# Kernel tuning notes

Hardware: AMD Instinct MI355X
Metric: run time of the kernel (lower is better)

Reference implementation:

```python
import jax, jax.numpy as jnp
import numpy as np

INF = 100000000.0
TOPK = 27


def _box_iou(a, b):
    # a: [N,4] (x1,y1,x2,y2), b: [G,4] -> iou [N,G]
    area_a = (a[:, 2] - a[:, 0]) * (a[:, 3] - a[:, 1])
    area_b = (b[:, 2] - b[:, 0]) * (b[:, 3] - b[:, 1])
    lt = jnp.maximum(a[:, None, :2], b[None, :, :2])
    rb = jnp.minimum(a[:, None, 2:], b[None, :, 2:])
    wh = jnp.clip(rb - lt, 0.0)
    inter = wh[..., 0] * wh[..., 1]
    union = area_a[:, None] + area_b[None, :] - inter
    return inter / union, union


def _assign_one(anchors, gts, tokens):
    # anchors [N,4], gts [G,4], tokens [G,T]
    N = anchors.shape[0]
    G = gts.shape[0]
    ious, _ = _box_iou(anchors, gts)  # [N,G]

    a_cx = (anchors[:, 2] + anchors[:, 0]) * 0.5
    a_cy = (anchors[:, 3] + anchors[:, 1]) * 0.5
    g_cx = (gts[:, 2] + gts[:, 0]) * 0.5
    g_cy = (gts[:, 3] + gts[:, 1]) * 0.5

    # pairwise center distance [N,G]
    dist = jnp.sqrt((a_cx[:, None] - g_cx[None, :]) ** 2 +
                    (a_cy[:, None] - g_cy[None, :]) ** 2)

    # topk nearest anchors per gt (smallest distance) -> idxs [G,TOPK]
    _, topk_idxs = jax.lax.top_k(-dist.T, TOPK)

    # candidate ious [G,TOPK]
    cand = jnp.take_along_axis(ious.T, topk_idxs, axis=1)
    iou_mean = cand.mean(axis=1)
    iou_std = cand.std(axis=1, ddof=1)  # torch.std is unbiased
    is_pos = cand >= (iou_mean + iou_std)[:, None]

    # center-inside-gt check [G,TOPK]
    ax = a_cx[topk_idxs]
    ay = a_cy[topk_idxs]
    l = ax - gts[:, 0:1]
    t = ay - gts[:, 1:2]
    r = gts[:, 2:3] - ax
    b = gts[:, 3:4] - ay
    is_in_gts = jnp.minimum(jnp.minimum(l, t), jnp.minimum(r, b)) > 0.01
    is_pos = is_pos & is_in_gts

    # scatter candidate ious into flat [G*N] buffer of -INF (indices are unique)
    flat_idx = (jnp.arange(G)[:, None] * N + topk_idxs).reshape(-1)
    vals = ious.T.reshape(-1)[flat_idx]
    scat = jnp.where(is_pos.reshape(-1), vals, -INF)
    ious_inf = jnp.full((G * N,), -INF, dtype=ious.dtype).at[flat_idx].set(scat)
    ious_inf = ious_inf.reshape(G, N).T  # [N,G]

    anchors_to_gt_values = ious_inf.max(axis=1)          # [N]
    anchors_to_gt_indexs = ious_inf.argmax(axis=1)       # [N]

    matched_gts = gts[anchors_to_gt_indexs]              # [N,4]

    T = tokens.shape[1]
    unmatched = jnp.zeros((T,), tokens.dtype).at[-1].set(1.0)
    token_labels = jnp.where((anchors_to_gt_values == -INF)[:, None],
                             unmatched[None, :],
                             tokens[anchors_to_gt_indexs])  # [N,T]
    return anchors_to_gt_values, anchors_to_gt_indexs, matched_gts, token_labels


def setup_inputs() -> dict:
    key = jax.random.key(0)
    k1, k2, k3, k4, k5 = jax.random.split(key, 5)
    B, N, G, T = 8, 100000, 64, 256
    # anchors: valid x1<x2, y1<y2 boxes on a ~1024px canvas
    a_c = jax.random.uniform(k1, (B, N, 2), jnp.float32, 0.0, 1024.0)
    a_wh = jax.random.uniform(k2, (B, N, 2), jnp.float32, 8.0, 128.0)
    anchor_boxes = jnp.concatenate([a_c - a_wh / 2, a_c + a_wh / 2], axis=-1)
    g_c = jax.random.uniform(k3, (B, G, 2), jnp.float32, 0.0, 1024.0)
    g_wh = jax.random.uniform(k4, (B, G, 2), jnp.float32, 64.0, 512.0)
    gt_boxes = jnp.concatenate([g_c - g_wh / 2, g_c + g_wh / 2], axis=-1)
    token_map = jax.random.uniform(k5, (B, G, T), jnp.float32)
    return {"anchor_boxes": anchor_boxes, "gt_boxes": gt_boxes,
            "token_map": token_map}


def reference(anchor_boxes, gt_boxes, token_map):
    return jax.vmap(_assign_one)(anchor_boxes, gt_boxes, token_map)
```

## Files before the change

kernel.cpp:

```cpp
#include <hip/hip_runtime.h>
#include <cstdint>

constexpr int B = 8, N = 100000, G = 64, T = 256, TOPK = 27;
constexpr int BN = B * N;
constexpr int CAP = 1536;
constexpr int GPB = 2;
constexpr int TOKEN_BLOCKS = 2048;
#define NEG_INF_VAL (-100000000.0f)

typedef float v4f __attribute__((ext_vector_type(4)));

__global__ __launch_bounds__(256) void atss_centers_kernel(
    const float* __restrict__ anchors, float2* __restrict__ ctr,
    unsigned long long* __restrict__ best)
{
#pragma clang fp contract(off)
  int i = blockIdx.x * 256 + threadIdx.x;
  if (i < BN) {
    float4 ab = ((const float4*)anchors)[i];
    ctr[i] = make_float2((ab.z + ab.x) * 0.5f, (ab.w + ab.y) * 0.5f);
    best[i] = 0ULL;
  }
}

__global__ __launch_bounds__(1024) void atss_assign_kernel(
    const float* __restrict__ anchors,
    const float2* __restrict__ ctr,
    const float* __restrict__ gts,
    unsigned long long* __restrict__ best)
{
#pragma clang fp contract(off)
  __shared__ float s_d[GPB][CAP];
  __shared__ int   s_i[GPB][CAP];
  __shared__ int   s_cnt[GPB];
  __shared__ int   s_sel[GPB][TOPK];
  __shared__ float s_iou[GPB][TOPK];
  __shared__ int   s_in[GPB][TOPK];
  __shared__ float s_thresh;

  const int bid = blockIdx.x;
  const int p   = (bid & 7) * 32 + (bid >> 3);
  const int b   = p >> 5;
  const int g0  = (p & 31) * 2;
  const int bg0 = b * G + g0;
  const int tid = threadIdx.x;

  const float4 gb0 = ((const float4*)gts)[bg0];
  const float4 gb1 = ((const float4*)gts)[bg0 + 1];
  const float gcx0 = (gb0.z + gb0.x) * 0.5f, gcy0 = (gb0.w + gb0.y) * 0.5f;
  const float gcx1 = (gb1.z + gb1.x) * 0.5f, gcy1 = (gb1.w + gb1.y) * 0.5f;

  const float4* abase = (const float4*)(anchors + (size_t)b * N * 4);
  const float4* c4    = (const float4*)(ctr + (size_t)b * N);

  float thr2_0 = 576.0f, thr2_1 = 576.0f;
  int M0 = -1, M1 = -1;
  for (int attempt = 0; attempt < 8 && (M0 < 0 || M1 < 0); ++attempt) {
    if (tid == 0 && M0 < 0) s_cnt[0] = 0;
    if (tid == 1 && M1 < 0) s_cnt[1] = 0;
    __syncthreads();
    const bool a0 = (M0 < 0), a1 = (M1 < 0);

#define ATSS_TEST(cx, cy, idx)                                                \
  do {                                                                        \
    if (a0) {                                                                 \
      float dx = (cx) - gcx0, dy = (cy) - gcy0;                               \
      float d2 = __fmul_rn(dx, dx) + __fmul_rn(dy, dy);                       \
      if (d2 < thr2_0) {                                                      \
        int q_ = atomicAdd(&s_cnt[0], 1);                                     \
        if (q_ < CAP) { s_d[0][q_] = __fsqrt_rn(d2); s_i[0][q_] = (idx); }    \
      }                                                                       \
    }                                                                         \
    if (a1) {                                                                 \
      float dx = (cx) - gcx1, dy = (cy) - gcy1;                               \
      float d2 = __fmul_rn(dx, dx) + __fmul_rn(dy, dy);                       \
      if (d2 < thr2_1) {                                                      \
        int q_ = atomicAdd(&s_cnt[1], 1);                                     \
        if (q_ < CAP) { s_d[1][q_] = __fsqrt_rn(d2); s_i[1][q_] = (idx); }    \
      }                                                                       \
    }                                                                         \
  } while (0)

    for (int m = tid; m < N / 4; m += 1024) {
      float4 ca = c4[2 * m];
      float4 cb = c4[2 * m + 1];
      ATSS_TEST(ca.x, ca.y, 4 * m);
      ATSS_TEST(ca.z, ca.w, 4 * m + 1);
      ATSS_TEST(cb.x, cb.y, 4 * m + 2);
      ATSS_TEST(cb.z, cb.w, 4 * m + 3);
    }
#undef ATSS_TEST
    __syncthreads();
    const int c0 = s_cnt[0], c1 = s_cnt[1];
    __syncthreads();
    if (M0 < 0) {
      if (c0 >= TOPK && c0 <= CAP) M0 = c0;
      else thr2_0 *= (c0 < TOPK) ? 16.0f : 0.25f;
    }
    if (M1 < 0) {
      if (c1 >= TOPK && c1 <= CAP) M1 = c1;
      else thr2_1 *= (c1 < TOPK) ? 16.0f : 0.25f;
    }
  }

  for (int q = 0; q < GPB; ++q) {
    const int M = (q == 0) ? M0 : M1;
    const float4 gbox = (q == 0) ? gb0 : gb1;
    const int g = g0 + q;

    for (int s = tid; s < M; s += 1024) {
      unsigned long long pk_s =
          ((unsigned long long)__float_as_uint(s_d[q][s]) << 20) |
          (unsigned long long)(unsigned)s_i[q][s];
      int rank = 0;
      for (int j = 0; j < M; ++j) {
        unsigned long long pk_j =
            ((unsigned long long)__float_as_uint(s_d[q][j]) << 20) |
            (unsigned long long)(unsigned)s_i[q][j];
        rank += (pk_j < pk_s) ? 1 : 0;
      }
      if (rank < TOPK) s_sel[q][rank] = s_i[q][s];
    }
    __syncthreads();

    if (tid < TOPK) {
      int a = s_sel[q][tid];
      float4 ab = abase[a];
      float area_a = __fmul_rn(ab.z - ab.x, ab.w - ab.y);
      float area_b = __fmul_rn(gbox.z - gbox.x, gbox.w - gbox.y);
      float ltx = fmaxf(ab.x, gbox.x), lty = fmaxf(ab.y, gbox.y);
      float rbx = fminf(ab.z, gbox.z), rby = fminf(ab.w, gbox.w);
      float w = fmaxf(rbx - ltx, 0.0f), h = fmaxf(rby - lty, 0.0f);
      float inter = __fmul_rn(w, h);
      float uni = (area_a + area_b) - inter;
      s_iou[q][tid] = inter / uni;
      float acx = (ab.z + ab.x) * 0.5f, acy = (ab.w + ab.y) * 0.5f;
      float l = acx - gbox.x, t = acy - gbox.y;
      float r = gbox.z - acx, bt = gbox.w - acy;
      float mn = fminf(fminf(l, t), fminf(r, bt));
      s_in[q][tid] = (mn > 0.01f) ? 1 : 0;
    }
    __syncthreads();

    if (tid == 0) {
      float sum = 0.0f;
      for (int k = 0; k < TOPK; ++k) sum += s_iou[q][k];
      float mean = sum / (float)TOPK;
      float vs = 0.0f;
      for (int k = 0; k < TOPK; ++k) {
        float d = s_iou[q][k] - mean;
        vs += __fmul_rn(d, d);
      }
      float sd = __fsqrt_rn(vs / (float)(TOPK - 1));
      s_thresh = mean + sd;
    }
    __syncthreads();

    if (tid < TOPK) {
      float iou = s_iou[q][tid];
      if (s_in[q][tid] && iou >= s_thresh) {
        unsigned long long pk =
            ((unsigned long long)__float_as_uint(iou) << 32) |
            (unsigned long long)(0xFFFFFFFFu - (unsigned)g);
        atomicMax(&best[(size_t)b * N + s_sel[q][tid]], pk);
      }
    }
    __syncthreads();
  }
}

__global__ __launch_bounds__(256) void atss_scalar_write_kernel(
    const unsigned long long* __restrict__ best,
    const float* __restrict__ gts,
    float* __restrict__ out)
{
  float* __restrict__ out_val = out;
  float* __restrict__ out_idx = out + (size_t)BN;
  float* __restrict__ out_mg  = out + (size_t)2 * BN;

  const int i = blockIdx.x * 256 + threadIdx.x;
  unsigned long long p = best[i];
  const int b_ = i / N;
  int g = 0;
  float val = NEG_INF_VAL;
  if (p != 0ULL) {
    g   = (int)(0xFFFFFFFFu - (unsigned)(p & 0xFFFFFFFFULL));
    val = __uint_as_float((unsigned)(p >> 32));
  }
  const int row = b_ * G + g;
  out_val[i] = val;
  out_idx[i] = (float)g;
  ((v4f*)out_mg)[i] = ((const v4f*)gts)[row];
}

__global__ __launch_bounds__(256) void atss_token_kernel(
    const unsigned long long* __restrict__ best,
    const float* __restrict__ tokens,
    float* __restrict__ out)
{
  float* __restrict__ out_tok = out + (size_t)6 * BN;
  const int lane = threadIdx.x & 63;
  const int NW   = TOKEN_BLOCKS * 4;
  int row = (blockIdx.x << 2) | (threadIdx.x >> 6);
  const v4f* tok4 = (const v4f*)tokens;

  unsigned long long p = best[row];
  while (true) {
    const int nrow = row + NW;
    unsigned long long pn = (nrow < BN) ? best[nrow] : 0ULL;
    v4f t;
    if (p != 0ULL) {
      const int b_ = row / N;
      const int g  = (int)(0xFFFFFFFFu - (unsigned)(p & 0xFFFFFFFFULL));
      t = tok4[(size_t)(b_ * G + g) * 64 + lane];
    } else {
      t = (v4f){0.0f, 0.0f, 0.0f, 0.0f};
      if (lane == 63) t.w = 1.0f;
    }
    ((v4f*)(out_tok + (size_t)row * T))[lane] = t;
    if (nrow >= BN) break;
    row = nrow;
    p = pn;
  }
}

extern "C" void kernel_launch(void* const* d_in, const int* in_sizes, int n_in,
                              void* d_out, int out_size, void* d_ws, size_t ws_size,
                              hipStream_t stream) {
  const float* anchors = (const float*)d_in[0];
  const float* gts     = (const float*)d_in[1];
  const float* tokens  = (const float*)d_in[2];
  float* out = (float*)d_out;

  unsigned long long* best = (unsigned long long*)d_ws;
  float2* ctr = (float2*)((char*)d_ws + sizeof(unsigned long long) * (size_t)BN);

  atss_centers_kernel<<<BN / 256, 256, 0, stream>>>(anchors, ctr, best);
  atss_assign_kernel<<<B * G / GPB, 1024, 0, stream>>>(anchors, ctr, gts, best);
  atss_scalar_write_kernel<<<BN / 256, 256, 0, stream>>>(best, gts, out);
  atss_token_kernel<<<TOKEN_BLOCKS, 256, 0, stream>>>(best, tokens, out);
}
```

Baseline: 853.4 us.

## Split token output into constant fill plus sparse worklist scatter; drop centers precompute

The token output is now written in two passes. A branch-free fill pass writes the unmatched one-hot pattern to every row, and a scatter pass copies token rows only for anchors on a worklist of positive assignments that the assign kernel appends through a global atomic counter. The separate centers kernel is also removed, and the assign kernel now computes anchor centers from the full anchor boxes, which doubles its scan reads. The scatter grid is sized for 16384 entries, and duplicate worklist entries are possible when one anchor is positive for several GTs.

New measurement: 861.5 us. About the same (+0.9%).

```diff
diff --git a/kernel.cpp b/kernel.cpp
--- a/kernel.cpp
+++ b/kernel.cpp
@@ -5,29 +5,26 @@
 constexpr int BN = B * N;
 constexpr int CAP = 1536;
 constexpr int GPB = 2;
-constexpr int TOKEN_BLOCKS = 2048;
+constexpr int WL_CAP = 16384;
+constexpr int FILL_BLOCKS = 2048;
 #define NEG_INF_VAL (-100000000.0f)
 
 typedef float v4f __attribute__((ext_vector_type(4)));
 
-__global__ __launch_bounds__(256) void atss_centers_kernel(
-    const float* __restrict__ anchors, float2* __restrict__ ctr,
-    unsigned long long* __restrict__ best)
-{
-#pragma clang fp contract(off)
+__global__ __launch_bounds__(256) void atss_zero_kernel(
+    unsigned long long* __restrict__ best, int* __restrict__ wl_cnt)
+{
   int i = blockIdx.x * 256 + threadIdx.x;
-  if (i < BN) {
-    float4 ab = ((const float4*)anchors)[i];
-    ctr[i] = make_float2((ab.z + ab.x) * 0.5f, (ab.w + ab.y) * 0.5f);
-    best[i] = 0ULL;
-  }
+  if (i < BN) best[i] = 0ULL;
+  if (i == 0) *wl_cnt = 0;
 }
 
 __global__ __launch_bounds__(1024) void atss_assign_kernel(
     const float* __restrict__ anchors,
-    const float2* __restrict__ ctr,
     const float* __restrict__ gts,
-    unsigned long long* __restrict__ best)
+    unsigned long long* __restrict__ best,
+    int* __restrict__ wl_cnt,
+    int* __restrict__ worklist)
 {
 #pragma clang fp contract(off)
   __shared__ float s_d[GPB][CAP];
@@ -51,7 +48,6 @@
   const float gcx1 = (gb1.z + gb1.x) * 0.5f, gcy1 = (gb1.w + gb1.y) * 0.5f;
 
   const float4* abase = (const float4*)(anchors + (size_t)b * N * 4);
-  const float4* c4    = (const float4*)(ctr + (size_t)b * N);
 
   float thr2_0 = 576.0f, thr2_1 = 576.0f;
   int M0 = -1, M1 = -1;
@@ -61,10 +57,12 @@
     __syncthreads();
     const bool a0 = (M0 < 0), a1 = (M1 < 0);
 
-#define ATSS_TEST(cx, cy, idx)                                                \
+#define ATSS_TEST(ab, idx)                                                    \
   do {                                                                        \
+    float cx = ((ab).z + (ab).x) * 0.5f;                                      \
+    float cy = ((ab).w + (ab).y) * 0.5f;                                      \
     if (a0) {                                                                 \
-      float dx = (cx) - gcx0, dy = (cy) - gcy0;                               \
+      float dx = cx - gcx0, dy = cy - gcy0;                                   \
       float d2 = __fmul_rn(dx, dx) + __fmul_rn(dy, dy);                       \
       if (d2 < thr2_0) {                                                      \
         int q_ = atomicAdd(&s_cnt[0], 1);                                     \
@@ -72,7 +70,7 @@
       }                                                                       \
     }                                                                         \
     if (a1) {                                                                 \
-      float dx = (cx) - gcx1, dy = (cy) - gcy1;                               \
+      float dx = cx - gcx1, dy = cy - gcy1;                                   \
       float d2 = __fmul_rn(dx, dx) + __fmul_rn(dy, dy);                       \
       if (d2 < thr2_1) {                                                      \
         int q_ = atomicAdd(&s_cnt[1], 1);                                     \
@@ -82,12 +80,14 @@
   } while (0)
 
     for (int m = tid; m < N / 4; m += 1024) {
-      float4 ca = c4[2 * m];
-      float4 cb = c4[2 * m + 1];
-      ATSS_TEST(ca.x, ca.y, 4 * m);
-      ATSS_TEST(ca.z, ca.w, 4 * m + 1);
-      ATSS_TEST(cb.x, cb.y, 4 * m + 2);
-      ATSS_TEST(cb.z, cb.w, 4 * m + 3);
+      float4 a0b = abase[4 * m];
+      float4 a1b = abase[4 * m + 1];
+      float4 a2b = abase[4 * m + 2];
+      float4 a3b = abase[4 * m + 3];
+      ATSS_TEST(a0b, 4 * m);
+      ATSS_TEST(a1b, 4 * m + 1);
+      ATSS_TEST(a2b, 4 * m + 2);
+      ATSS_TEST(a3b, 4 * m + 3);
     }
 #undef ATSS_TEST
     __syncthreads();
@@ -158,11 +158,21 @@
 
     if (tid < TOPK) {
       float iou = s_iou[q][tid];
-      if (s_in[q][tid] && iou >= s_thresh) {
+      bool pos = s_in[q][tid] && (iou >= s_thresh);
+      if (pos) {
         unsigned long long pk =
             ((unsigned long long)__float_as_uint(iou) << 32) |
             (unsigned long long)(0xFFFFFFFFu - (unsigned)g);
         atomicMax(&best[(size_t)b * N + s_sel[q][tid]], pk);
+      }
+      unsigned long long mask = __ballot(pos);
+      int nact = __popcll(mask);
+      int base = 0;
+      if (tid == 0 && nact > 0) base = atomicAdd(wl_cnt, nact);
+      base = __shfl(base, 0);
+      if (pos) {
+        int rank = __popcll(mask & ((1ULL << tid) - 1ULL));
+        worklist[base + rank] = b * N + s_sel[q][tid];
       }
     }
     __syncthreads();
@@ -193,35 +203,35 @@
   ((v4f*)out_mg)[i] = ((const v4f*)gts)[row];
 }
 
-__global__ __launch_bounds__(256) void atss_token_kernel(
+__global__ __launch_bounds__(256) void atss_token_fill_kernel(
+    float* __restrict__ out)
+{
+  v4f* __restrict__ tok = (v4f*)(out + (size_t)6 * BN);
+  const int NT = FILL_BLOCKS * 256;
+  const int total = BN * (T / 4);
+  for (int j = blockIdx.x * 256 + threadIdx.x; j < total; j += NT) {
+    v4f t = (v4f){0.0f, 0.0f, 0.0f, ((j & 63) == 63) ? 1.0f : 0.0f};
+    tok[j] = t;
+  }
+}
+
+__global__ __launch_bounds__(256) void atss_token_scatter_kernel(
     const unsigned long long* __restrict__ best,
+    const int* __restrict__ wl_cnt,
+    const int* __restrict__ worklist,
     const float* __restrict__ tokens,
     float* __restrict__ out)
 {
-  float* __restrict__ out_tok = out + (size_t)6 * BN;
+  const int w = blockIdx.x * 4 + (threadIdx.x >> 6);
   const int lane = threadIdx.x & 63;
-  const int NW   = TOKEN_BLOCKS * 4;
-  int row = (blockIdx.x << 2) | (threadIdx.x >> 6);
-  const v4f* tok4 = (const v4f*)tokens;
-
-  unsigned long long p = best[row];
-  while (true) {
-    const int nrow = row + NW;
-    unsigned long long pn = (nrow < BN) ? best[nrow] : 0ULL;
-    v4f t;
-    if (p != 0ULL) {
-      const int b_ = row / N;
-      const int g  = (int)(0xFFFFFFFFu - (unsigned)(p & 0xFFFFFFFFULL));
-      t = tok4[(size_t)(b_ * G + g) * 64 + lane];
-    } else {
-      t = (v4f){0.0f, 0.0f, 0.0f, 0.0f};
-      if (lane == 63) t.w = 1.0f;
-    }
-    ((v4f*)(out_tok + (size_t)row * T))[lane] = t;
-    if (nrow >= BN) break;
-    row = nrow;
-    p = pn;
-  }
+  const int cnt = *wl_cnt;
+  if (w >= cnt) return;
+  const int i = worklist[w];
+  const unsigned long long p = best[i];
+  const int b_ = i / N;
+  const int g  = (int)(0xFFFFFFFFu - (unsigned)(p & 0xFFFFFFFFULL));
+  v4f t = ((const v4f*)tokens)[(size_t)(b_ * G + g) * 64 + lane];
+  ((v4f*)(out + (size_t)6 * BN + (size_t)i * T))[lane] = t;
 }
 
 extern "C" void kernel_launch(void* const* d_in, const int* in_sizes, int n_in,
@@ -233,10 +243,14 @@
   float* out = (float*)d_out;
 
   unsigned long long* best = (unsigned long long*)d_ws;
-  float2* ctr = (float2*)((char*)d_ws + sizeof(unsigned long long) * (size_t)BN);
-
-  atss_centers_kernel<<<BN / 256, 256, 0, stream>>>(anchors, ctr, best);
-  atss_assign_kernel<<<B * G / GPB, 1024, 0, stream>>>(anchors, ctr, gts, best);
+  int* wl_cnt   = (int*)((char*)d_ws + sizeof(unsigned long long) * (size_t)BN);
+  int* worklist = wl_cnt + 16;
+
+  atss_zero_kernel<<<(BN + 255) / 256, 256, 0, stream>>>(best, wl_cnt);
+  atss_assign_kernel<<<B * G / GPB, 1024, 0, stream>>>(anchors, gts, best,
+                                                       wl_cnt, worklist);
   atss_scalar_write_kernel<<<BN / 256, 256, 0, stream>>>(best, gts, out);
-  atss_token_kernel<<<TOKEN_BLOCKS, 256, 0, stream>>>(best, tokens, out);
-}
+  atss_token_fill_kernel<<<FILL_BLOCKS, 256, 0, stream>>>(out);
+  atss_token_scatter_kernel<<<(WL_CAP + 1023) / 1024 * 256, 256, 0, stream>>>(
+      best, wl_cnt, worklist, tokens, out);
+}
```
